# Optimization experiments

Hardware: AMD Instinct MI355X
Metric: run time of the kernel (lower is better)

The kernel has to match this reference:

```python
import jax, jax.numpy as jnp
import numpy as np

EPS = 1e-5

def _mvn(feat):
    # instance-norm style mean/std over spatial dims; torch .var is unbiased (ddof=1)
    b, c = feat.shape[:2]
    flat = feat.reshape(b, c, -1)
    mu = flat.mean(-1)[:, :, None, None]
    std = jnp.sqrt(flat.var(-1, ddof=1) + EPS)[:, :, None, None]
    return (feat - mu) / std

def setup_inputs() -> dict:
    key = jax.random.key(0)
    ks = jax.random.split(key, 10)
    B, C, H, W = 4, 512, 64, 64
    sc = 0.05
    return {
        "content": jax.random.normal(ks[0], (B, C, H, W), jnp.float32),
        "style": jax.random.normal(ks[1], (B, C, H, W), jnp.float32),
        "content_key": jax.random.normal(ks[2], (B, C, H, W), jnp.float32),
        "style_key": jax.random.normal(ks[3], (B, C, H, W), jnp.float32),
        "Wf": jax.random.normal(ks[4], (C, C), jnp.float32) * sc,
        "bf": jax.random.normal(ks[5], (C,), jnp.float32) * sc,
        "Wg": jax.random.normal(ks[6], (C, C), jnp.float32) * sc,
        "bg": jax.random.normal(ks[7], (C,), jnp.float32) * sc,
        "Wh": jax.random.normal(ks[8], (C, C), jnp.float32) * sc,
        "bh": jax.random.normal(ks[9], (C,), jnp.float32) * sc,
    }

def reference(content, style, content_key, style_key, Wf, bf, Wg, bg, Wh, bh):
    b, C, h, w = content.shape
    hs, ws = style.shape[2], style.shape[3]
    n, m = h * w, hs * ws
    # 1x1 convs are per-pixel linear maps
    Fq = jnp.einsum('oc,bcn->bno', Wf, content_key.reshape(b, -1, n)) + bf      # [b, n, ck]
    G = jnp.einsum('oc,bcn->bon', Wg, style_key.reshape(b, -1, m)) + bg[:, None]  # [b, ck, m]
    V = jnp.einsum('oc,bcn->bno', Wh, style.reshape(b, C, m)) + bh              # [b, m, C]
    S = jax.nn.softmax(jnp.einsum('bnc,bcm->bnm', Fq, G), axis=-1)              # [b, n, m]
    mean = jnp.einsum('bnm,bmc->bnc', S, V)                                     # attention-weighted mean
    m2 = jnp.einsum('bnm,bmc->bnc', S, V * V)                                   # weighted second moment
    std = jnp.sqrt(jax.nn.relu(m2 - mean * mean))
    mean = mean.reshape(b, h, w, C).transpose(0, 3, 1, 2)
    std = std.reshape(b, h, w, C).transpose(0, 3, 1, 2)
    return std * _mvn(content) + mean
```

## Files before the change

### kernel.cpp

```cpp
#include <hip/hip_runtime.h>
#include <math.h>

#define BATCH 4
#define C 512
#define N 4096
#define M 4096
#define MSPLIT 4

typedef __attribute__((ext_vector_type(8))) short short8;
typedef __attribute__((ext_vector_type(8))) __bf16 bf16x8;
typedef __attribute__((ext_vector_type(4))) float f32x4;

static __device__ __forceinline__ unsigned short f2bf(float x) {
    unsigned u = __float_as_uint(x);
    u += 0x7fff + ((u >> 16) & 1);
    return (unsigned short)(u >> 16);
}
static __device__ __forceinline__ float bf2f(unsigned short h) {
    return __uint_as_float(((unsigned)h) << 16);
}
static __device__ __forceinline__ f32x4 mfma_bf16(short8 a, short8 b, f32x4 c) {
    return __builtin_amdgcn_mfma_f32_16x16x32_bf16(
        __builtin_bit_cast(bf16x8, a), __builtin_bit_cast(bf16x8, b), c, 0, 0, 0);
}

__global__ __launch_bounds__(256) void wsplit_kernel(
    const float* __restrict__ W, unsigned short* __restrict__ hi,
    unsigned short* __restrict__ lo)
{
    int i = blockIdx.x * 256 + threadIdx.x;
    float v = W[i];
    unsigned short h = f2bf(v);
    hi[i] = h;
    lo[i] = f2bf(v - bf2f(h));
}

__global__ __launch_bounds__(256) void linear_fg_mfma(
    const float* __restrict__ in,
    const unsigned short* __restrict__ Whi, const unsigned short* __restrict__ Wlo,
    const float* __restrict__ bias,
    unsigned short* __restrict__ out_hi, unsigned short* __restrict__ out_lo)
{
    __shared__ float in_s[32][68];
    __shared__ __align__(16) unsigned short wh_s[64][40];
    __shared__ __align__(16) unsigned short wl_s[64][40];
    const int tid = threadIdx.x;
    const int n0 = blockIdx.x * 64, o0 = blockIdx.y * 64;
    const int w = tid >> 6, lane = tid & 63;
    const int wrow = w >> 1, wcol = w & 1;
    const int lr = lane & 15, q = lane >> 4;
    f32x4 acc[2][2];
    #pragma unroll
    for (int i = 0; i < 2; ++i)
        #pragma unroll
        for (int j = 0; j < 2; ++j) acc[i][j] = (f32x4){0.f, 0.f, 0.f, 0.f};

    for (int kc = 0; kc < C; kc += 32) {
        __syncthreads();
        #pragma unroll
        for (int it = 0; it < 2; ++it) {
            int idx = tid + it * 256;
            int k = idx >> 4, seg = idx & 15;
            *(float4*)&in_s[k][seg * 4] =
                *(const float4*)&in[(size_t)(kc + k) * N + n0 + seg * 4];
        }
        {
            int o = tid >> 2, sg = tid & 3;
            *(float4*)&wh_s[o][sg * 8] = *(const float4*)&Whi[(size_t)(o0 + o) * 512 + kc + sg * 8];
            *(float4*)&wl_s[o][sg * 8] = *(const float4*)&Wlo[(size_t)(o0 + o) * 512 + kc + sg * 8];
        }
        __syncthreads();
        short8 ah[2], al[2], bh[2], bl[2];
        #pragma unroll
        for (int i = 0; i < 2; ++i) {
            int n = wrow * 32 + i * 16 + lr;
            #pragma unroll
            for (int j = 0; j < 8; ++j) {
                float f = in_s[q * 8 + j][n];
                unsigned short h = f2bf(f);
                ah[i][j] = (short)h;
                al[i][j] = (short)f2bf(f - bf2f(h));
            }
        }
        #pragma unroll
        for (int j = 0; j < 2; ++j) {
            int o = wcol * 32 + j * 16 + lr;
            bh[j] = *(const short8*)&wh_s[o][q * 8];
            bl[j] = *(const short8*)&wl_s[o][q * 8];
        }
        #pragma unroll
        for (int i = 0; i < 2; ++i)
            #pragma unroll
            for (int j = 0; j < 2; ++j) {
                acc[i][j] = mfma_bf16(ah[i], bh[j], acc[i][j]);
                acc[i][j] = mfma_bf16(ah[i], bl[j], acc[i][j]);
                acc[i][j] = mfma_bf16(al[i], bh[j], acc[i][j]);
            }
    }
    #pragma unroll
    for (int i = 0; i < 2; ++i)
        #pragma unroll
        for (int j = 0; j < 2; ++j) {
            int o = o0 + wcol * 32 + j * 16 + lr;
            float bo = bias[o];
            #pragma unroll
            for (int r = 0; r < 4; ++r) {
                int n = n0 + wrow * 32 + i * 16 + q * 4 + r;
                float v = acc[i][j][r] + bo;
                unsigned short h = f2bf(v);
                out_hi[(size_t)n * 512 + o] = h;
                out_lo[(size_t)n * 512 + o] = f2bf(v - bf2f(h));
            }
        }
}

__global__ __launch_bounds__(256) void linear_v_mfma(
    const float* __restrict__ in,
    const unsigned short* __restrict__ Whi, const unsigned short* __restrict__ Wlo,
    const float* __restrict__ bias,
    unsigned short* __restrict__ vhT, unsigned short* __restrict__ v2hT,
    unsigned short* __restrict__ v2lT)
{
    __shared__ float in_s[32][68];
    __shared__ __align__(16) unsigned short wh_s[64][40];
    __shared__ __align__(16) unsigned short wl_s[64][40];
    const int tid = threadIdx.x;
    const int m0 = blockIdx.x * 64, o0 = blockIdx.y * 64;
    const int w = tid >> 6, lane = tid & 63;
    const int wrow = w >> 1, wcol = w & 1;
    const int lr = lane & 15, q = lane >> 4;
    f32x4 acc[2][2];
    #pragma unroll
    for (int i = 0; i < 2; ++i)
        #pragma unroll
        for (int j = 0; j < 2; ++j) acc[i][j] = (f32x4){0.f, 0.f, 0.f, 0.f};

    for (int kc = 0; kc < C; kc += 32) {
        __syncthreads();
        #pragma unroll
        for (int it = 0; it < 2; ++it) {
            int idx = tid + it * 256;
            int k = idx >> 4, seg = idx & 15;
            *(float4*)&in_s[k][seg * 4] =
                *(const float4*)&in[(size_t)(kc + k) * N + m0 + seg * 4];
        }
        {
            int o = tid >> 2, sg = tid & 3;
            *(float4*)&wh_s[o][sg * 8] = *(const float4*)&Whi[(size_t)(o0 + o) * 512 + kc + sg * 8];
            *(float4*)&wl_s[o][sg * 8] = *(const float4*)&Wlo[(size_t)(o0 + o) * 512 + kc + sg * 8];
        }
        __syncthreads();
        short8 ah[2], al[2], bh[2], bl[2];
        #pragma unroll
        for (int i = 0; i < 2; ++i) {
            int o = wrow * 32 + i * 16 + lr;
            ah[i] = *(const short8*)&wh_s[o][q * 8];
            al[i] = *(const short8*)&wl_s[o][q * 8];
        }
        #pragma unroll
        for (int j = 0; j < 2; ++j) {
            int m = wcol * 32 + j * 16 + lr;
            #pragma unroll
            for (int t = 0; t < 8; ++t) {
                float f = in_s[q * 8 + t][m];
                unsigned short h = f2bf(f);
                bh[j][t] = (short)h;
                bl[j][t] = (short)f2bf(f - bf2f(h));
            }
        }
        #pragma unroll
        for (int i = 0; i < 2; ++i)
            #pragma unroll
            for (int j = 0; j < 2; ++j) {
                acc[i][j] = mfma_bf16(ah[i], bh[j], acc[i][j]);
                acc[i][j] = mfma_bf16(ah[i], bl[j], acc[i][j]);
                acc[i][j] = mfma_bf16(al[i], bh[j], acc[i][j]);
            }
    }
    #pragma unroll
    for (int i = 0; i < 2; ++i)
        #pragma unroll
        for (int r = 0; r < 4; ++r) {
            int o = o0 + wrow * 32 + i * 16 + q * 4 + r;
            float bo = bias[o];
            #pragma unroll
            for (int j = 0; j < 2; ++j) {
                int m = m0 + wcol * 32 + j * 16 + lr;
                float v = acc[i][j][r] + bo;
                unsigned short vh = f2bf(v);
                float vhf = bf2f(vh);
                float vsq = vhf * vhf;
                unsigned short v2h = f2bf(vsq);
                unsigned short v2l = f2bf(vsq - bf2f(v2h));
                size_t off = (size_t)o * M + m;
                vhT[off] = vh;
                v2hT[off] = v2h;
                v2lT[off] = v2l;
            }
        }
}

__global__ __launch_bounds__(256) void logits_mfma_kernel(
    const unsigned short* __restrict__ Ah, const unsigned short* __restrict__ Al,
    const unsigned short* __restrict__ Bh, const unsigned short* __restrict__ Bl,
    float* __restrict__ S)
{
    __shared__ __align__(16) unsigned short Ah_s[128 * 40];
    __shared__ __align__(16) unsigned short Al_s[128 * 40];
    __shared__ __align__(16) unsigned short Bh_s[128 * 40];
    __shared__ __align__(16) unsigned short Bl_s[128 * 40];
    const int tid = threadIdx.x;
    const int n0 = blockIdx.y * 128, m0 = blockIdx.x * 128;
    const int w = tid >> 6, lane = tid & 63;
    const int wrow = w >> 1, wcol = w & 1;
    const int lr = lane & 15, q = lane >> 4;
    f32x4 acc[4][4];
    #pragma unroll
    for (int i = 0; i < 4; ++i)
        #pragma unroll
        for (int j = 0; j < 4; ++j)
            acc[i][j] = (f32x4){0.f, 0.f, 0.f, 0.f};

    for (int kc = 0; kc < C; kc += 32) {
        __syncthreads();
        #pragma unroll
        for (int it = 0; it < 2; ++it) {
            int idx = tid + it * 256;
            int row = idx >> 2, seg = idx & 3;
            int ldso = row * 40 + seg * 8;
            int go = kc + seg * 8;
            *(float4*)&Ah_s[ldso] = *(const float4*)&Ah[(size_t)(n0 + row) * C + go];
            *(float4*)&Al_s[ldso] = *(const float4*)&Al[(size_t)(n0 + row) * C + go];
            *(float4*)&Bh_s[ldso] = *(const float4*)&Bh[(size_t)(m0 + row) * C + go];
            *(float4*)&Bl_s[ldso] = *(const float4*)&Bl[(size_t)(m0 + row) * C + go];
        }
        __syncthreads();
        short8 ah[4], al[4], bh[4], bl[4];
        #pragma unroll
        for (int i = 0; i < 4; ++i) {
            int ro = (wrow * 64 + i * 16 + lr) * 40 + q * 8;
            int co = (wcol * 64 + i * 16 + lr) * 40 + q * 8;
            ah[i] = *(const short8*)&Ah_s[ro];
            al[i] = *(const short8*)&Al_s[ro];
            bh[i] = *(const short8*)&Bh_s[co];
            bl[i] = *(const short8*)&Bl_s[co];
        }
        #pragma unroll
        for (int i = 0; i < 4; ++i)
            #pragma unroll
            for (int j = 0; j < 4; ++j) {
                acc[i][j] = mfma_bf16(ah[i], bh[j], acc[i][j]);
                acc[i][j] = mfma_bf16(ah[i], bl[j], acc[i][j]);
                acc[i][j] = mfma_bf16(al[i], bh[j], acc[i][j]);
            }
    }
    #pragma unroll
    for (int i = 0; i < 4; ++i) {
        int nb = n0 + wrow * 64 + i * 16 + q * 4;
        #pragma unroll
        for (int j = 0; j < 4; ++j) {
            int m = m0 + wcol * 64 + j * 16 + lr;
            #pragma unroll
            for (int r = 0; r < 4; ++r)
                S[(size_t)(nb + r) * M + m] = acc[i][j][r];
        }
    }
}

__global__ __launch_bounds__(256) void rowstat_p_kernel(
    const float* __restrict__ S, unsigned short* __restrict__ P,
    float* __restrict__ rsum)
{
    const int n = blockIdx.x;
    const int tid = threadIdx.x;
    const float* row = S + (size_t)n * M;
    float v[16];
    #pragma unroll
    for (int i = 0; i < 16; ++i) v[i] = row[tid + i * 256];
    float lm = -INFINITY;
    #pragma unroll
    for (int i = 0; i < 16; ++i) lm = fmaxf(lm, v[i]);
    #pragma unroll
    for (int off = 32; off > 0; off >>= 1) lm = fmaxf(lm, __shfl_xor(lm, off, 64));
    __shared__ float red[4];
    __shared__ float redsum[4];
    const int wid = tid >> 6, lane = tid & 63;
    if (lane == 0) red[wid] = lm;
    __syncthreads();
    const float rm = fmaxf(fmaxf(red[0], red[1]), fmaxf(red[2], red[3]));
    float ls = 0.f;
    unsigned short* prow = P + (size_t)n * M;
    #pragma unroll
    for (int i = 0; i < 16; ++i) {
        float p = __expf(v[i] - rm);
        unsigned short pb = f2bf(p);
        prow[tid + i * 256] = pb;
        ls += bf2f(pb);
    }
    #pragma unroll
    for (int off = 32; off > 0; off >>= 1) ls += __shfl_xor(ls, off, 64);
    if (lane == 0) redsum[wid] = ls;
    __syncthreads();
    if (tid == 0) rsum[n] = redsum[0] + redsum[1] + redsum[2] + redsum[3];
}

__global__ __launch_bounds__(256) void apply_partial_kernel(
    const unsigned short* __restrict__ P, const unsigned short* __restrict__ VhT,
    const unsigned short* __restrict__ V2hT, const unsigned short* __restrict__ V2lT,
    float* __restrict__ accm_p, float* __restrict__ acc2_p)
{
    __shared__ __align__(16) unsigned short P_s[128 * 40];
    __shared__ __align__(16) unsigned short Vh_s[64 * 40];
    __shared__ __align__(16) unsigned short V2h_s[64 * 40];
    __shared__ __align__(16) unsigned short V2l_s[64 * 40];
    const int tid = threadIdx.x;
    const int c0 = blockIdx.x * 64, n0 = blockIdx.y * 128;
    const int z = blockIdx.z;
    const int w = tid >> 6, lane = tid & 63;
    const int wrow = w >> 1, wcol = w & 1;
    const int lr = lane & 15, q = lane >> 4;
    f32x4 accm[4][2], acc2[4][2];
    #pragma unroll
    for (int i = 0; i < 4; ++i)
        #pragma unroll
        for (int j = 0; j < 2; ++j) {
            accm[i][j] = (f32x4){0.f, 0.f, 0.f, 0.f};
            acc2[i][j] = (f32x4){0.f, 0.f, 0.f, 0.f};
        }

    const int mbeg = z * (M / MSPLIT);
    for (int mc = mbeg; mc < mbeg + M / MSPLIT; mc += 32) {
        __syncthreads();
        #pragma unroll
        for (int it = 0; it < 2; ++it) {
            int idx = tid + it * 256;
            int row = idx >> 2, seg = idx & 3;
            *(float4*)&P_s[row * 40 + seg * 8] =
                *(const float4*)&P[(size_t)(n0 + row) * M + mc + seg * 8];
        }
        {
            int row = tid >> 2, seg = tid & 3;
            int ldso = row * 40 + seg * 8;
            size_t go = (size_t)(c0 + row) * M + mc + seg * 8;
            *(float4*)&Vh_s[ldso]  = *(const float4*)&VhT[go];
            *(float4*)&V2h_s[ldso] = *(const float4*)&V2hT[go];
            *(float4*)&V2l_s[ldso] = *(const float4*)&V2lT[go];
        }
        __syncthreads();
        short8 a[4], bmat[2], b2h[2], b2l[2];
        #pragma unroll
        for (int i = 0; i < 4; ++i)
            a[i] = *(const short8*)&P_s[(wrow * 64 + i * 16 + lr) * 40 + q * 8];
        #pragma unroll
        for (int j = 0; j < 2; ++j) {
            int co = (wcol * 32 + j * 16 + lr) * 40 + q * 8;
            bmat[j] = *(const short8*)&Vh_s[co];
            b2h[j]  = *(const short8*)&V2h_s[co];
            b2l[j]  = *(const short8*)&V2l_s[co];
        }
        #pragma unroll
        for (int i = 0; i < 4; ++i)
            #pragma unroll
            for (int j = 0; j < 2; ++j) {
                accm[i][j] = mfma_bf16(a[i], bmat[j], accm[i][j]);
                acc2[i][j] = mfma_bf16(a[i], b2h[j],  acc2[i][j]);
                acc2[i][j] = mfma_bf16(a[i], b2l[j],  acc2[i][j]);
            }
    }
    const size_t pbase = (size_t)z * N * C;
    #pragma unroll
    for (int i = 0; i < 4; ++i) {
        int nb = n0 + wrow * 64 + i * 16 + q * 4;
        #pragma unroll
        for (int j = 0; j < 2; ++j) {
            int c = c0 + wcol * 32 + j * 16 + lr;
            #pragma unroll
            for (int r = 0; r < 4; ++r) {
                size_t off = pbase + (size_t)(nb + r) * C + c;
                accm_p[off] = accm[i][j][r];
                acc2_p[off] = acc2[i][j][r];
            }
        }
    }
}

__global__ __launch_bounds__(256) void combine_kernel(
    const float* __restrict__ accm_p, const float* __restrict__ acc2_p,
    const float* __restrict__ rsum, float* __restrict__ meanw,
    float* __restrict__ stdw)
{
    const size_t idx = ((size_t)blockIdx.x * 256 + threadIdx.x) * 4;
    const int n = (int)(idx >> 9);
    const float inv = 1.0f / rsum[n];
    float sm[4] = {0.f, 0.f, 0.f, 0.f}, s2[4] = {0.f, 0.f, 0.f, 0.f};
    #pragma unroll
    for (int z = 0; z < MSPLIT; ++z) {
        float4 a = *(const float4*)&accm_p[(size_t)z * N * C + idx];
        float4 b = *(const float4*)&acc2_p[(size_t)z * N * C + idx];
        sm[0] += a.x; sm[1] += a.y; sm[2] += a.z; sm[3] += a.w;
        s2[0] += b.x; s2[1] += b.y; s2[2] += b.z; s2[3] += b.w;
    }
    float4 mnv, sdv;
    float* mp = (float*)&mnv;
    float* sp = (float*)&sdv;
    #pragma unroll
    for (int k = 0; k < 4; ++k) {
        float mn = sm[k] * inv;
        float m2 = s2[k] * inv;
        mp[k] = mn;
        sp[k] = sqrtf(fmaxf(m2 - mn * mn, 0.f));
    }
    *(float4*)&meanw[idx] = mnv;
    *(float4*)&stdw[idx]  = sdv;
}

__global__ __launch_bounds__(256) void mvn_kernel(
    const float* __restrict__ content, float* __restrict__ mu, float* __restrict__ rstd)
{
    const int c = blockIdx.x;
    const int tid = threadIdx.x;
    const float* row = content + (size_t)c * N;
    float s = 0.f, ss = 0.f;
    for (int i = tid; i < N; i += 256) {
        float v = row[i];
        s += v;
        ss = fmaf(v, v, ss);
    }
    #pragma unroll
    for (int off = 32; off > 0; off >>= 1) {
        s  += __shfl_xor(s,  off, 64);
        ss += __shfl_xor(ss, off, 64);
    }
    __shared__ float rs[4], rss[4];
    const int wid = tid >> 6, lane = tid & 63;
    if (lane == 0) { rs[wid] = s; rss[wid] = ss; }
    __syncthreads();
    if (tid == 0) {
        float st = rs[0] + rs[1] + rs[2] + rs[3];
        float sst = rss[0] + rss[1] + rss[2] + rss[3];
        float m = st / (float)N;
        float var = (sst - st * st / (float)N) / (float)(N - 1);
        mu[c] = m;
        rstd[c] = rsqrtf(var + 1e-5f);
    }
}

__global__ __launch_bounds__(256) void final_kernel(
    const float* __restrict__ content, const float* __restrict__ meanw,
    const float* __restrict__ stdw, const float* __restrict__ mu,
    const float* __restrict__ rstd, float* __restrict__ out)
{
    __shared__ float mn_s[32][33], sd_s[32][33];
    const int tid = threadIdx.x;
    const int n0 = blockIdx.x * 32;
    const int c0 = blockIdx.y * 32;
    const int tx = tid & 31, ty = tid >> 5;
    #pragma unroll
    for (int i = 0; i < 4; ++i) {
        int n = ty + i * 8;
        mn_s[tx][n] = meanw[(size_t)(n0 + n) * C + c0 + tx];
        sd_s[tx][n] = stdw [(size_t)(n0 + n) * C + c0 + tx];
    }
    __syncthreads();
    #pragma unroll
    for (int i = 0; i < 4; ++i) {
        int c = ty + i * 8;
        float m = mu[c0 + c], r = rstd[c0 + c];
        size_t off = (size_t)(c0 + c) * N + n0 + tx;
        float x = content[off];
        out[off] = sd_s[c][tx] * (x - m) * r + mn_s[c][tx];
    }
}

extern "C" void kernel_launch(void* const* d_in, const int* in_sizes, int n_in,
                              void* d_out, int out_size, void* d_ws, size_t ws_size,
                              hipStream_t stream)
{
    const float* content = (const float*)d_in[0];
    const float* style   = (const float*)d_in[1];
    const float* ckey    = (const float*)d_in[2];
    const float* skey    = (const float*)d_in[3];
    const float* Wf      = (const float*)d_in[4];
    const float* bf      = (const float*)d_in[5];
    const float* Wg      = (const float*)d_in[6];
    const float* bg      = (const float*)d_in[7];
    const float* Wh      = (const float*)d_in[8];
    const float* bh      = (const float*)d_in[9];
    float* out = (float*)d_out;

    const size_t sz_w  = (size_t)512 * 512 * 2;
    const size_t sz_S  = (size_t)N * M * 4;
    const size_t sz_FG = (size_t)N * C * 2;
    const size_t sz_P  = (size_t)N * M * 2;
    const size_t sz_V  = (size_t)C * M * 2;

    char* p = (char*)d_ws;
    auto alloc = [&](size_t bytes) {
        char* r = p;
        p += (bytes + 255) & ~(size_t)255;
        return r;
    };
    unsigned short* WfH = (unsigned short*)alloc(sz_w);
    unsigned short* WfL = (unsigned short*)alloc(sz_w);
    unsigned short* WgH = (unsigned short*)alloc(sz_w);
    unsigned short* WgL = (unsigned short*)alloc(sz_w);
    unsigned short* WhH = (unsigned short*)alloc(sz_w);
    unsigned short* WhL = (unsigned short*)alloc(sz_w);
    float* S = (float*)alloc(sz_S);
    unsigned short* Fh = (unsigned short*)alloc(sz_FG);
    unsigned short* Fl = (unsigned short*)alloc(sz_FG);
    unsigned short* Gh = (unsigned short*)alloc(sz_FG);
    unsigned short* Gl = (unsigned short*)alloc(sz_FG);
    unsigned short* P    = (unsigned short*)alloc(sz_P);
    unsigned short* VhT  = (unsigned short*)alloc(sz_V);
    unsigned short* V2hT = (unsigned short*)alloc(sz_V);
    unsigned short* V2lT = (unsigned short*)alloc(sz_V);
    float* rsum  = (float*)alloc((size_t)N * 4);
    float* meanw = (float*)alloc((size_t)N * C * 4);
    float* stdw  = (float*)alloc((size_t)N * C * 4);
    float* mu    = (float*)alloc((size_t)C * 4);
    float* rstd  = (float*)alloc((size_t)C * 4);

    float* accm_p = S;
    float* acc2_p = S + (size_t)MSPLIT * N * C;

    wsplit_kernel<<<dim3(1024), 256, 0, stream>>>(Wf, WfH, WfL);
    wsplit_kernel<<<dim3(1024), 256, 0, stream>>>(Wg, WgH, WgL);
    wsplit_kernel<<<dim3(1024), 256, 0, stream>>>(Wh, WhH, WhL);

    for (int b = 0; b < BATCH; ++b) {
        const size_t fo = (size_t)b * C * N;
        linear_fg_mfma<<<dim3(N / 64, C / 64), 256, 0, stream>>>(ckey + fo, WfH, WfL, bf, Fh, Fl);
        linear_fg_mfma<<<dim3(M / 64, C / 64), 256, 0, stream>>>(skey + fo, WgH, WgL, bg, Gh, Gl);
        linear_v_mfma<<<dim3(M / 64, C / 64), 256, 0, stream>>>(style + fo, WhH, WhL, bh,
                                                                VhT, V2hT, V2lT);
        logits_mfma_kernel<<<dim3(M / 128, N / 128), 256, 0, stream>>>(Fh, Fl, Gh, Gl, S);
        rowstat_p_kernel<<<dim3(N), 256, 0, stream>>>(S, P, rsum);
        apply_partial_kernel<<<dim3(C / 64, N / 128, MSPLIT), 256, 0, stream>>>(
            P, VhT, V2hT, V2lT, accm_p, acc2_p);
        combine_kernel<<<dim3(N * C / 1024), 256, 0, stream>>>(
            accm_p, acc2_p, rsum, meanw, stdw);
        mvn_kernel<<<dim3(C), 256, 0, stream>>>(content + fo, mu, rstd);
        final_kernel<<<dim3(N / 32, C / 32), 256, 0, stream>>>(
            content + fo, meanw, stdw, mu, rstd, out + fo);
    }
}
```

Before: 1.148 ms.

## Load MFMA operands directly from global memory, bypassing LDS staging

In the logits kernel the A (query) operands are now read straight from global memory into registers in MFMA fragment layout instead of going through shared memory. The apply kernel drops LDS entirely and instead software-pipelines direct global loads of P and the V operands with two register buffers, overlapping the next chunk's loads with the current MFMAs. This removes LDS traffic and barriers but makes the global reads less coalesced (16-byte strided row segments) and drops cross-wave reuse, relying on L1/L2 hits instead.

```diff
diff --git a/kernel.cpp b/kernel.cpp
--- a/kernel.cpp
+++ b/kernel.cpp
@@ -205,8 +205,6 @@
     const unsigned short* __restrict__ Bh, const unsigned short* __restrict__ Bl,
     float* __restrict__ S)
 {
-    __shared__ __align__(16) unsigned short Ah_s[128 * 40];
-    __shared__ __align__(16) unsigned short Al_s[128 * 40];
     __shared__ __align__(16) unsigned short Bh_s[128 * 40];
     __shared__ __align__(16) unsigned short Bl_s[128 * 40];
     const int tid = threadIdx.x;
@@ -214,6 +212,16 @@
     const int w = tid >> 6, lane = tid & 63;
     const int wrow = w >> 1, wcol = w & 1;
     const int lr = lane & 15, q = lane >> 4;
+
+    const unsigned short* ahp[4];
+    const unsigned short* alp[4];
+    #pragma unroll
+    for (int i = 0; i < 4; ++i) {
+        size_t ro = (size_t)(n0 + wrow * 64 + i * 16 + lr) * C + q * 8;
+        ahp[i] = Ah + ro;
+        alp[i] = Al + ro;
+    }
+
     f32x4 acc[4][4];
     #pragma unroll
     for (int i = 0; i < 4; ++i)
@@ -229,21 +237,22 @@
             int row = idx >> 2, seg = idx & 3;
             int ldso = row * 40 + seg * 8;
             int go = kc + seg * 8;
-            *(float4*)&Ah_s[ldso] = *(const float4*)&Ah[(size_t)(n0 + row) * C + go];
-            *(float4*)&Al_s[ldso] = *(const float4*)&Al[(size_t)(n0 + row) * C + go];
             *(float4*)&Bh_s[ldso] = *(const float4*)&Bh[(size_t)(m0 + row) * C + go];
             *(float4*)&Bl_s[ldso] = *(const float4*)&Bl[(size_t)(m0 + row) * C + go];
         }
+        short8 ah[4], al[4];
+        #pragma unroll
+        for (int i = 0; i < 4; ++i) {
+            ah[i] = *(const short8*)(ahp[i] + kc);
+            al[i] = *(const short8*)(alp[i] + kc);
+        }
         __syncthreads();
-        short8 ah[4], al[4], bh[4], bl[4];
-        #pragma unroll
-        for (int i = 0; i < 4; ++i) {
-            int ro = (wrow * 64 + i * 16 + lr) * 40 + q * 8;
-            int co = (wcol * 64 + i * 16 + lr) * 40 + q * 8;
-            ah[i] = *(const short8*)&Ah_s[ro];
-            al[i] = *(const short8*)&Al_s[ro];
-            bh[i] = *(const short8*)&Bh_s[co];
-            bl[i] = *(const short8*)&Bl_s[co];
+        short8 bh[4], bl[4];
+        #pragma unroll
+        for (int j = 0; j < 4; ++j) {
+            int co = (wcol * 64 + j * 16 + lr) * 40 + q * 8;
+            bh[j] = *(const short8*)&Bh_s[co];
+            bl[j] = *(const short8*)&Bl_s[co];
         }
         #pragma unroll
         for (int i = 0; i < 4; ++i)
@@ -309,16 +318,27 @@
     const unsigned short* __restrict__ V2hT, const unsigned short* __restrict__ V2lT,
     float* __restrict__ accm_p, float* __restrict__ acc2_p)
 {
-    __shared__ __align__(16) unsigned short P_s[128 * 40];
-    __shared__ __align__(16) unsigned short Vh_s[64 * 40];
-    __shared__ __align__(16) unsigned short V2h_s[64 * 40];
-    __shared__ __align__(16) unsigned short V2l_s[64 * 40];
     const int tid = threadIdx.x;
     const int c0 = blockIdx.x * 64, n0 = blockIdx.y * 128;
     const int z = blockIdx.z;
     const int w = tid >> 6, lane = tid & 63;
     const int wrow = w >> 1, wcol = w & 1;
     const int lr = lane & 15, q = lane >> 4;
+    const int mbeg = z * (M / MSPLIT);
+
+    const unsigned short* ap[4];
+    #pragma unroll
+    for (int i = 0; i < 4; ++i)
+        ap[i] = P + (size_t)(n0 + wrow * 64 + i * 16 + lr) * M + mbeg + q * 8;
+    const unsigned short* bp[6];
+    #pragma unroll
+    for (int j = 0; j < 2; ++j) {
+        size_t ro = (size_t)(c0 + wcol * 32 + j * 16 + lr) * M + mbeg + q * 8;
+        bp[j]     = VhT  + ro;
+        bp[2 + j] = V2hT + ro;
+        bp[4 + j] = V2lT + ro;
+    }
+
     f32x4 accm[4][2], acc2[4][2];
     #pragma unroll
     for (int i = 0; i < 4; ++i)
@@ -328,45 +348,45 @@
             acc2[i][j] = (f32x4){0.f, 0.f, 0.f, 0.f};
         }
 
-    const int mbeg = z * (M / MSPLIT);
-    for (int mc = mbeg; mc < mbeg + M / MSPLIT; mc += 32) {
-        __syncthreads();
-        #pragma unroll
-        for (int it = 0; it < 2; ++it) {
-            int idx = tid + it * 256;
-            int row = idx >> 2, seg = idx & 3;
-            *(float4*)&P_s[row * 40 + seg * 8] =
-                *(const float4*)&P[(size_t)(n0 + row) * M + mc + seg * 8];
-        }
-        {
-            int row = tid >> 2, seg = tid & 3;
-            int ldso = row * 40 + seg * 8;
-            size_t go = (size_t)(c0 + row) * M + mc + seg * 8;
-            *(float4*)&Vh_s[ldso]  = *(const float4*)&VhT[go];
-            *(float4*)&V2h_s[ldso] = *(const float4*)&V2hT[go];
-            *(float4*)&V2l_s[ldso] = *(const float4*)&V2lT[go];
-        }
-        __syncthreads();
-        short8 a[4], bmat[2], b2h[2], b2l[2];
+    auto do_mfma = [&](const short8 (&a)[4], const short8 (&b)[6]) {
         #pragma unroll
         for (int i = 0; i < 4; ++i)
-            a[i] = *(const short8*)&P_s[(wrow * 64 + i * 16 + lr) * 40 + q * 8];
-        #pragma unroll
-        for (int j = 0; j < 2; ++j) {
-            int co = (wcol * 32 + j * 16 + lr) * 40 + q * 8;
-            bmat[j] = *(const short8*)&Vh_s[co];
-            b2h[j]  = *(const short8*)&V2h_s[co];
-            b2l[j]  = *(const short8*)&V2l_s[co];
-        }
-        #pragma unroll
-        for (int i = 0; i < 4; ++i)
             #pragma unroll
             for (int j = 0; j < 2; ++j) {
-                accm[i][j] = mfma_bf16(a[i], bmat[j], accm[i][j]);
-                acc2[i][j] = mfma_bf16(a[i], b2h[j],  acc2[i][j]);
-                acc2[i][j] = mfma_bf16(a[i], b2l[j],  acc2[i][j]);
-            }
-    }
+                accm[i][j] = mfma_bf16(a[i], b[j],     accm[i][j]);
+                acc2[i][j] = mfma_bf16(a[i], b[2 + j], acc2[i][j]);
+                acc2[i][j] = mfma_bf16(a[i], b[4 + j], acc2[i][j]);
+            }
+    };
+
+    short8 fa[4], fb[6], ga[4], gb[6];
+    #pragma unroll
+    for (int i = 0; i < 4; ++i) fa[i] = *(const short8*)ap[i];
+    #pragma unroll
+    for (int j = 0; j < 6; ++j) fb[j] = *(const short8*)bp[j];
+
+    #pragma unroll 1
+    for (int it = 0; it < 15; ++it) {
+        const int off1 = it * 64 + 32;
+        const int off2 = it * 64 + 64;
+        #pragma unroll
+        for (int i = 0; i < 4; ++i) ga[i] = *(const short8*)(ap[i] + off1);
+        #pragma unroll
+        for (int j = 0; j < 6; ++j) gb[j] = *(const short8*)(bp[j] + off1);
+        do_mfma(fa, fb);
+        #pragma unroll
+        for (int i = 0; i < 4; ++i) fa[i] = *(const short8*)(ap[i] + off2);
+        #pragma unroll
+        for (int j = 0; j < 6; ++j) fb[j] = *(const short8*)(bp[j] + off2);
+        do_mfma(ga, gb);
+    }
+    #pragma unroll
+    for (int i = 0; i < 4; ++i) ga[i] = *(const short8*)(ap[i] + 992);
+    #pragma unroll
+    for (int j = 0; j < 6; ++j) gb[j] = *(const short8*)(bp[j] + 992);
+    do_mfma(fa, fb);
+    do_mfma(ga, gb);
+
     const size_t pbase = (size_t)z * N * C;
     #pragma unroll
     for (int i = 0; i < 4; ++i) {
```

Measured after the change: 1.498 ms. +30.5%, slower.
